# Kernel optimization log

Hardware: AMD Instinct MI355X
Metric: run time of the kernel (lower is better)

Reference implementation:

```python
import jax, jax.numpy as jnp
import numpy as np

N_NODES = 100000
N_EDGES = 3200000
N_GRAPHS = 64
IN_DIM = 64
LATENT = 64
DIST_STD = 1.0


def _gcn_conv(x, W, b, src, dst, dinv):
    """PyG GCNConv: out = D^-1/2 (A+I) D^-1/2 (x W) + b, with dinv = deg^-1/2."""
    n = x.shape[0]
    h = x @ W  # [N, out]
    coef = dinv[src] * dinv[dst]  # per-edge norm
    agg = jax.ops.segment_sum(h[src] * coef[:, None], dst, num_segments=n)
    # self-loop contribution with norm dinv[i]^2
    return agg + h * (dinv * dinv)[:, None] + b


def _mean_pool(x, batch, num_graphs):
    sums = jax.ops.segment_sum(x, batch, num_segments=num_graphs)
    cnts = jax.ops.segment_sum(jnp.ones((x.shape[0],), x.dtype), batch, num_segments=num_graphs)
    return sums / jnp.maximum(cnts, 1.0)[:, None]


def setup_inputs() -> dict:
    key = jax.random.key(0)
    ks = jax.random.split(key, 12)
    x = jax.random.normal(ks[0], (N_NODES, IN_DIM), jnp.float32)
    edge_index = jax.random.randint(ks[1], (2, N_EDGES), 0, N_NODES, jnp.int64 if jax.config.jax_enable_x64 else jnp.int32).astype(jnp.int32)
    batch = jnp.sort(jax.random.randint(ks[2], (N_NODES,), 0, N_GRAPHS)).astype(jnp.int32)

    def glorot(k, shape):
        fan_in, fan_out = shape
        s = jnp.sqrt(6.0 / (fan_in + fan_out))
        return jax.random.uniform(k, shape, jnp.float32, -s, s)

    return {
        "x": x, "edge_index": edge_index, "batch": batch,
        "W1m": glorot(ks[3], (IN_DIM, 16)), "b1m": jnp.zeros((16,), jnp.float32),
        "W2m": glorot(ks[4], (16, 32)), "b2m": jnp.zeros((32,), jnp.float32),
        "W3m": glorot(ks[5], (32, LATENT)), "b3m": jnp.zeros((LATENT,), jnp.float32),
        "W1l": glorot(ks[6], (IN_DIM, 16)), "b1l": jnp.zeros((16,), jnp.float32),
        "W2l": glorot(ks[7], (16, 32)), "b2l": jnp.zeros((32,), jnp.float32),
        "W3l": glorot(ks[8], (32, LATENT)), "b3l": jnp.zeros((LATENT,), jnp.float32),
        "Wfc": glorot(ks[9], (LATENT, 160000)), "bfc": jnp.zeros((160000,), jnp.float32),
        "eps": jax.random.normal(ks[10], (N_GRAPHS, LATENT), jnp.float32) * DIST_STD,
    }


def reference(x, edge_index, batch, W1m, b1m, W2m, b2m, W3m, b3m,
              W1l, b1l, W2l, b2l, W3l, b3l, Wfc, bfc, eps):
    src, dst = edge_index[0], edge_index[1]
    n = x.shape[0]
    # degrees include self-loop (+1)
    deg = jax.ops.segment_sum(jnp.ones((src.shape[0],), x.dtype), dst, num_segments=n) + 1.0
    dinv = jax.lax.rsqrt(deg)

    mu = jax.nn.relu(_gcn_conv(x, W1m, b1m, src, dst, dinv))
    mu = jax.nn.relu(_gcn_conv(mu, W2m, b2m, src, dst, dinv))
    mu = jax.nn.relu(_gcn_conv(mu, W3m, b3m, src, dst, dinv))
    mu = _mean_pool(mu, batch, N_GRAPHS)

    log = jax.nn.relu(_gcn_conv(x, W1l, b1l, src, dst, dinv))
    log = jax.nn.relu(_gcn_conv(log, W2l, b2l, src, dst, dinv))
    log = jax.nn.relu(_gcn_conv(log, W3l, b3l, src, dst, dinv))
    logvar = _mean_pool(log, batch, N_GRAPHS)

    # latent sample (training mode): z = mu + eps * exp(0.5*logvar)
    z = mu + eps * jnp.exp(0.5 * logvar)

    # decode: sigmoid(z Wfc + bfc) -> [G, 400, 400]
    output = jax.nn.sigmoid(z @ Wfc + bfc).reshape(-1, 400, 400)
    return output, mu, logvar
```

## Files before the change

### kernel.cpp

```cpp
#include <hip/hip_runtime.h>
#include <hip/hip_bf16.h>

#define N_NODES 100000
#define N_EDGES 3200000
#define N_GRAPHS 64
#define NB 391
#define KCH 8192
#define NCHUNK ((N_EDGES + KCH - 1) / KCH)
#define MAXBKT 10240
#define NBLK3 (N_NODES / 32)

__device__ __forceinline__ void atomAddF(float* p, float v) {
    unsafeAtomicAdd(p, v);
}

__device__ __forceinline__ float lo2f(unsigned u) { return __uint_as_float(u << 16); }
__device__ __forceinline__ float hi2f(unsigned u) { return __uint_as_float(u & 0xFFFF0000u); }
__device__ __forceinline__ unsigned pack2(float a, float b) {
    unsigned ha = __bfloat16_as_ushort(__float2bfloat16(a));
    unsigned hb = __bfloat16_as_ushort(__float2bfloat16(b));
    return ha | (hb << 16);
}

__global__ __launch_bounds__(512) void k_binCount(const int* __restrict__ dst,
                                                  int* __restrict__ gcount) {
    __shared__ int hist[NB];
    for (int t = threadIdx.x; t < NB; t += 512) hist[t] = 0;
    __syncthreads();
    int base = blockIdx.x * KCH;
    int cnt = min(KCH, N_EDGES - base);
    for (int i = threadIdx.x; i < cnt; i += 512)
        atomicAdd(&hist[dst[base + i] >> 8], 1);
    __syncthreads();
    for (int t = threadIdx.x; t < NB; t += 512)
        if (hist[t]) atomicAdd(&gcount[t], hist[t]);
}

__global__ __launch_bounds__(512) void k_scanB(const int* __restrict__ gcount,
                                               int* __restrict__ gbase,
                                               int* __restrict__ gcursor,
                                               int* __restrict__ rowptr) {
    __shared__ int s[512];
    int v = (threadIdx.x < NB) ? gcount[threadIdx.x] : 0;
    s[threadIdx.x] = v;
    __syncthreads();
    for (int off = 1; off < 512; off <<= 1) {
        int t = (threadIdx.x >= off) ? s[threadIdx.x - off] : 0;
        __syncthreads();
        s[threadIdx.x] += t;
        __syncthreads();
    }
    if (threadIdx.x < NB) {
        int e = s[threadIdx.x] - v;
        gbase[threadIdx.x] = e;
        gcursor[threadIdx.x] = e;
    }
    if (threadIdx.x == 0) rowptr[N_NODES] = N_EDGES;
}

__global__ __launch_bounds__(512) void k_binA(const int* __restrict__ src,
                                              const int* __restrict__ dst,
                                              int* __restrict__ gcursor,
                                              int* __restrict__ binned) {
    __shared__ int hist[512];
    __shared__ int rbase[512];
    hist[threadIdx.x] = 0;
    __syncthreads();
    int base = blockIdx.x * KCH;
    int cnt = min(KCH, N_EDGES - base);
    int pk[16];
    int meta[16];
    #pragma unroll
    for (int i = 0; i < 16; ++i) {
        int idx = i * 512 + threadIdx.x;
        if (idx < cnt) {
            int d = dst[base + idx];
            int b = d >> 8;
            int pos = atomicAdd(&hist[b], 1);
            pk[i] = ((d & 255) << 24) | src[base + idx];
            meta[i] = (b << 13) | pos;
        } else {
            meta[i] = -1;
        }
    }
    __syncthreads();
    if (threadIdx.x < NB) {
        int v = hist[threadIdx.x];
        if (v > 0) rbase[threadIdx.x] = atomicAdd(&gcursor[threadIdx.x], v);
    }
    __syncthreads();
    #pragma unroll
    for (int i = 0; i < 16; ++i) {
        if (meta[i] >= 0) {
            int b = meta[i] >> 13;
            int pos = meta[i] & 8191;
            binned[rbase[b] + pos] = pk[i];
        }
    }
}

__global__ __launch_bounds__(512) void k_passB(const int* __restrict__ gbase,
                                               int* __restrict__ csr,
                                               int* __restrict__ rowptr,
                                               float* __restrict__ dinv) {
    int b = blockIdx.x;
    int rb = gbase[b];
    int re = (b == NB - 1) ? N_EDGES : gbase[b + 1];
    int cnt = re - rb;
    int nbase = b << 8;
    int nn = min(nbase + 256, N_NODES) - nbase;
    __shared__ int stage[MAXBKT];
    __shared__ int nhist[256];
    __shared__ int sc[256];
    __shared__ int ncur[256];
    for (int t = threadIdx.x; t < 256; t += 512) nhist[t] = 0;
    __syncthreads();
    for (int j = threadIdx.x; j < cnt; j += 512) {
        int p = csr[rb + j];
        stage[j] = p;
        atomicAdd(&nhist[((unsigned)p) >> 24], 1);
    }
    __syncthreads();
    if (threadIdx.x < 256) sc[threadIdx.x] = nhist[threadIdx.x];
    __syncthreads();
    for (int off = 1; off < 256; off <<= 1) {
        int t = (threadIdx.x < 256 && threadIdx.x >= off) ? sc[threadIdx.x - off] : 0;
        __syncthreads();
        if (threadIdx.x < 256) sc[threadIdx.x] += t;
        __syncthreads();
    }
    if (threadIdx.x < 256) {
        int e = sc[threadIdx.x] - nhist[threadIdx.x];
        ncur[threadIdx.x] = e;
        if (threadIdx.x < nn) {
            rowptr[nbase + threadIdx.x] = rb + e;
            dinv[nbase + threadIdx.x] = rsqrtf((float)nhist[threadIdx.x] + 1.0f);
        }
    }
    __syncthreads();
    for (int j = threadIdx.x; j < cnt; j += 512) {
        int p = stage[j];
        int slot = atomicAdd(&ncur[((unsigned)p) >> 24], 1);
        csr[rb + slot] = p;
    }
}

template<int LOGW, bool BIAS_RELU, bool OB, bool PRE>
__global__ void __launch_bounds__(256) k_gatherB(
        const int* __restrict__ rowptr, const int* __restrict__ csr,
        const unsigned* __restrict__ in ,
        const float* __restrict__ dinv,
        const float* __restrict__ ba, const float* __restrict__ bb,
        void* __restrict__ out) {
    constexpr int W8 = (1 << LOGW) / 8;
    constexpr int NPB = 256 / W8;
    int n = blockIdx.x * NPB + (threadIdx.x / W8);
    if (n >= N_NODES) return;
    int sub = threadIdx.x % W8;
    const uint4* in4 = (const uint4*)in;
    uint4 u = in4[(size_t)n * W8 + sub];
    float a0 = lo2f(u.x), a1 = hi2f(u.x), a2 = lo2f(u.y), a3 = hi2f(u.y);
    float a4 = lo2f(u.z), a5 = hi2f(u.z), a6 = lo2f(u.w), a7 = hi2f(u.w);
    int j = rowptr[n], end = rowptr[n + 1];
    for (; j + 8 <= end; j += 8) {
        int s0 = csr[j] & 0xFFFFFF;
        int s1 = csr[j + 1] & 0xFFFFFF;
        int s2 = csr[j + 2] & 0xFFFFFF;
        int s3 = csr[j + 3] & 0xFFFFFF;
        int s4 = csr[j + 4] & 0xFFFFFF;
        int s5 = csr[j + 5] & 0xFFFFFF;
        int s6 = csr[j + 6] & 0xFFFFFF;
        int s7 = csr[j + 7] & 0xFFFFFF;
        uint4 v0 = in4[(size_t)s0 * W8 + sub];
        uint4 v1 = in4[(size_t)s1 * W8 + sub];
        uint4 v2 = in4[(size_t)s2 * W8 + sub];
        uint4 v3 = in4[(size_t)s3 * W8 + sub];
        uint4 v4 = in4[(size_t)s4 * W8 + sub];
        uint4 v5 = in4[(size_t)s5 * W8 + sub];
        uint4 v6 = in4[(size_t)s6 * W8 + sub];
        uint4 v7 = in4[(size_t)s7 * W8 + sub];
        a0 += ((lo2f(v0.x) + lo2f(v1.x)) + (lo2f(v2.x) + lo2f(v3.x)))
            + ((lo2f(v4.x) + lo2f(v5.x)) + (lo2f(v6.x) + lo2f(v7.x)));
        a1 += ((hi2f(v0.x) + hi2f(v1.x)) + (hi2f(v2.x) + hi2f(v3.x)))
            + ((hi2f(v4.x) + hi2f(v5.x)) + (hi2f(v6.x) + hi2f(v7.x)));
        a2 += ((lo2f(v0.y) + lo2f(v1.y)) + (lo2f(v2.y) + lo2f(v3.y)))
            + ((lo2f(v4.y) + lo2f(v5.y)) + (lo2f(v6.y) + lo2f(v7.y)));
        a3 += ((hi2f(v0.y) + hi2f(v1.y)) + (hi2f(v2.y) + hi2f(v3.y)))
            + ((hi2f(v4.y) + hi2f(v5.y)) + (hi2f(v6.y) + hi2f(v7.y)));
        a4 += ((lo2f(v0.z) + lo2f(v1.z)) + (lo2f(v2.z) + lo2f(v3.z)))
            + ((lo2f(v4.z) + lo2f(v5.z)) + (lo2f(v6.z) + lo2f(v7.z)));
        a5 += ((hi2f(v0.z) + hi2f(v1.z)) + (hi2f(v2.z) + hi2f(v3.z)))
            + ((hi2f(v4.z) + hi2f(v5.z)) + (hi2f(v6.z) + hi2f(v7.z)));
        a6 += ((lo2f(v0.w) + lo2f(v1.w)) + (lo2f(v2.w) + lo2f(v3.w)))
            + ((lo2f(v4.w) + lo2f(v5.w)) + (lo2f(v6.w) + lo2f(v7.w)));
        a7 += ((hi2f(v0.w) + hi2f(v1.w)) + (hi2f(v2.w) + hi2f(v3.w)))
            + ((hi2f(v4.w) + hi2f(v5.w)) + (hi2f(v6.w) + hi2f(v7.w)));
    }
    for (; j < end; ++j) {
        int s = csr[j] & 0xFFFFFF;
        uint4 v = in4[(size_t)s * W8 + sub];
        a0 += lo2f(v.x); a1 += hi2f(v.x);
        a2 += lo2f(v.y); a3 += hi2f(v.y);
        a4 += lo2f(v.z); a5 += hi2f(v.z);
        a6 += lo2f(v.w); a7 += hi2f(v.w);
    }
    float di = dinv[n];
    a0 *= di; a1 *= di; a2 *= di; a3 *= di;
    a4 *= di; a5 *= di; a6 *= di; a7 *= di;
    if (BIAS_RELU) {
        constexpr int H = (1 << LOGW) / 2;
        int d = sub * 8;
        const float* bp = (d < H) ? (ba + d) : (bb + d - H);
        a0 = fmaxf(a0 + bp[0], 0.0f);
        a1 = fmaxf(a1 + bp[1], 0.0f);
        a2 = fmaxf(a2 + bp[2], 0.0f);
        a3 = fmaxf(a3 + bp[3], 0.0f);
        a4 = fmaxf(a4 + bp[4], 0.0f);
        a5 = fmaxf(a5 + bp[5], 0.0f);
        a6 = fmaxf(a6 + bp[6], 0.0f);
        a7 = fmaxf(a7 + bp[7], 0.0f);
    }
    if (PRE) {
        a0 *= di; a1 *= di; a2 *= di; a3 *= di;
        a4 *= di; a5 *= di; a6 *= di; a7 *= di;
    }
    if (OB) {
        ((uint4*)out)[(size_t)n * W8 + sub] =
            make_uint4(pack2(a0, a1), pack2(a2, a3), pack2(a4, a5), pack2(a6, a7));
    } else {
        constexpr int OUT4 = (1 << LOGW) / 4;
        float4* o4 = (float4*)out;
        o4[(size_t)n * OUT4 + sub * 2]     = make_float4(a0, a1, a2, a3);
        o4[(size_t)n * OUT4 + sub * 2 + 1] = make_float4(a4, a5, a6, a7);
    }
}

#define FMA4(A, W) \
    A.x = fmaf(r, W.x, A.x); A.y = fmaf(r, W.y, A.y); \
    A.z = fmaf(r, W.z, A.z); A.w = fmaf(r, W.w, A.w);

__global__ void __launch_bounds__(256) k_gd3(
        const int* __restrict__ rowptr, const int* __restrict__ csr,
        const unsigned* __restrict__ in,
        const float* __restrict__ dinv,
        const float* __restrict__ W3m, const float* __restrict__ b3m,
        const float* __restrict__ W3l, const float* __restrict__ b3l,
        const int* __restrict__ batch,
        float* __restrict__ part0, float* __restrict__ part1,
        int* __restrict__ pg0, int* __restrict__ pg1, int boff) {
    __shared__ float s_ali[32 * 160];
    __shared__ float agg[32 * 68];
    __shared__ float sbias[128];
    __shared__ int   sbatch[32];
    __shared__ int   ssplit;
    float* sWall = s_ali;
    float* h3s   = s_ali;

    int blk = blockIdx.x + boff;
    for (int t = threadIdx.x; t < 4096; t += 256) {
        int k = t >> 7, D = t & 127;
        float wv = (D < 64) ? W3m[k * 64 + D] : W3l[k * 64 + (D - 64)];
        sWall[k * 160 + (D >> 4) * 20 + (D & 15)] = wv;
    }
    if (threadIdx.x < 128)
        sbias[threadIdx.x] = (threadIdx.x < 64) ? b3m[threadIdx.x]
                                                : b3l[threadIdx.x - 64];
    int nbase = blk * 32;
    if (threadIdx.x < 32) sbatch[threadIdx.x] = batch[nbase + threadIdx.x];

    int ln  = threadIdx.x >> 3;
    int sub = threadIdx.x & 7;
    int n = nbase + ln;
    const uint4* in4 = (const uint4*)in;
    uint4 u = in4[(size_t)n * 8 + sub];
    float a0 = lo2f(u.x), a1 = hi2f(u.x), a2 = lo2f(u.y), a3 = hi2f(u.y);
    float a4 = lo2f(u.z), a5 = hi2f(u.z), a6 = lo2f(u.w), a7 = hi2f(u.w);
    int j = rowptr[n], end = rowptr[n + 1];
    for (; j + 8 <= end; j += 8) {
        int s0 = csr[j] & 0xFFFFFF;
        int s1 = csr[j + 1] & 0xFFFFFF;
        int s2 = csr[j + 2] & 0xFFFFFF;
        int s3 = csr[j + 3] & 0xFFFFFF;
        int s4 = csr[j + 4] & 0xFFFFFF;
        int s5 = csr[j + 5] & 0xFFFFFF;
        int s6 = csr[j + 6] & 0xFFFFFF;
        int s7 = csr[j + 7] & 0xFFFFFF;
        uint4 v0 = in4[(size_t)s0 * 8 + sub];
        uint4 v1 = in4[(size_t)s1 * 8 + sub];
        uint4 v2 = in4[(size_t)s2 * 8 + sub];
        uint4 v3 = in4[(size_t)s3 * 8 + sub];
        uint4 v4 = in4[(size_t)s4 * 8 + sub];
        uint4 v5 = in4[(size_t)s5 * 8 + sub];
        uint4 v6 = in4[(size_t)s6 * 8 + sub];
        uint4 v7 = in4[(size_t)s7 * 8 + sub];
        a0 += ((lo2f(v0.x) + lo2f(v1.x)) + (lo2f(v2.x) + lo2f(v3.x)))
            + ((lo2f(v4.x) + lo2f(v5.x)) + (lo2f(v6.x) + lo2f(v7.x)));
        a1 += ((hi2f(v0.x) + hi2f(v1.x)) + (hi2f(v2.x) + hi2f(v3.x)))
            + ((hi2f(v4.x) + hi2f(v5.x)) + (hi2f(v6.x) + hi2f(v7.x)));
        a2 += ((lo2f(v0.y) + lo2f(v1.y)) + (lo2f(v2.y) + lo2f(v3.y)))
            + ((lo2f(v4.y) + lo2f(v5.y)) + (lo2f(v6.y) + lo2f(v7.y)));
        a3 += ((hi2f(v0.y) + hi2f(v1.y)) + (hi2f(v2.y) + hi2f(v3.y)))
            + ((hi2f(v4.y) + hi2f(v5.y)) + (hi2f(v6.y) + hi2f(v7.y)));
        a4 += ((lo2f(v0.z) + lo2f(v1.z)) + (lo2f(v2.z) + lo2f(v3.z)))
            + ((lo2f(v4.z) + lo2f(v5.z)) + (lo2f(v6.z) + lo2f(v7.z)));
        a5 += ((hi2f(v0.z) + hi2f(v1.z)) + (hi2f(v2.z) + hi2f(v3.z)))
            + ((hi2f(v4.z) + hi2f(v5.z)) + (hi2f(v6.z) + hi2f(v7.z)));
        a6 += ((lo2f(v0.w) + lo2f(v1.w)) + (lo2f(v2.w) + lo2f(v3.w)))
            + ((lo2f(v4.w) + lo2f(v5.w)) + (lo2f(v6.w) + lo2f(v7.w)));
        a7 += ((hi2f(v0.w) + hi2f(v1.w)) + (hi2f(v2.w) + hi2f(v3.w)))
            + ((hi2f(v4.w) + hi2f(v5.w)) + (hi2f(v6.w) + hi2f(v7.w)));
    }
    for (; j < end; ++j) {
        int s = csr[j] & 0xFFFFFF;
        uint4 v = in4[(size_t)s * 8 + sub];
        a0 += lo2f(v.x); a1 += hi2f(v.x);
        a2 += lo2f(v.y); a3 += hi2f(v.y);
        a4 += lo2f(v.z); a5 += hi2f(v.z);
        a6 += lo2f(v.w); a7 += hi2f(v.w);
    }
    float di = dinv[n];
    a0 *= di; a1 *= di; a2 *= di; a3 *= di;
    a4 *= di; a5 *= di; a6 *= di; a7 *= di;
    {
        float* ap = &agg[ln * 68 + sub * 8];
        *(float4*)&ap[0] = make_float4(a0, a1, a2, a3);
        *(float4*)&ap[4] = make_float4(a4, a5, a6, a7);
    }
    if (threadIdx.x == 0) {
        int sp = 32;
        int ga = sbatch[0];
        for (int i = 1; i < 32; ++i)
            if (sbatch[i] != ga) { sp = i; break; }
        ssplit = sp;
    }
    __syncthreads();

    int ln2 = threadIdx.x >> 3;
    int q   = threadIdx.x & 7;
    int Dbase = q * 16;
    int koff = (q >= 4) ? 32 : 0;
    float4 c0 = *(const float4*)&sbias[Dbase];
    float4 c1 = *(const float4*)&sbias[Dbase + 4];
    float4 c2 = *(const float4*)&sbias[Dbase + 8];
    float4 c3 = *(const float4*)&sbias[Dbase + 12];
    const float* ag = &agg[ln2 * 68 + koff];
    const float* wq = &sWall[q * 20];
    #pragma unroll
    for (int k = 0; k < 32; ++k) {
        float r = ag[k];
        const float* wr = &wq[k * 160];
        float4 w0 = *(const float4*)&wr[0];
        float4 w1 = *(const float4*)&wr[4];
        float4 w2 = *(const float4*)&wr[8];
        float4 w3 = *(const float4*)&wr[12];
        FMA4(c0, w0)
        FMA4(c1, w1)
        FMA4(c2, w2)
        FMA4(c3, w3)
    }
    c0.x = fmaxf(c0.x, 0.f); c0.y = fmaxf(c0.y, 0.f);
    c0.z = fmaxf(c0.z, 0.f); c0.w = fmaxf(c0.w, 0.f);
    c1.x = fmaxf(c1.x, 0.f); c1.y = fmaxf(c1.y, 0.f);
    c1.z = fmaxf(c1.z, 0.f); c1.w = fmaxf(c1.w, 0.f);
    c2.x = fmaxf(c2.x, 0.f); c2.y = fmaxf(c2.y, 0.f);
    c2.z = fmaxf(c2.z, 0.f); c2.w = fmaxf(c2.w, 0.f);
    c3.x = fmaxf(c3.x, 0.f); c3.y = fmaxf(c3.y, 0.f);
    c3.z = fmaxf(c3.z, 0.f); c3.w = fmaxf(c3.w, 0.f);
    __syncthreads();

    {
        float* hp = &h3s[ln2 * 132 + Dbase];
        *(float4*)&hp[0]  = c0;
        *(float4*)&hp[4]  = c1;
        *(float4*)&hp[8]  = c2;
        *(float4*)&hp[12] = c3;
    }
    __syncthreads();
    {
        int d    = threadIdx.x & 127;
        int slot = threadIdx.x >> 7;
        int sp = ssplit;
        int s = slot ? sp : 0;
        int e = slot ? 32 : sp;
        float acc = 0.f;
        for (int nn = s; nn < e; ++nn)
            acc += h3s[nn * 132 + d];
        if (slot == 0) {
            part0[(size_t)blk * 128 + d] = acc;
            if (d == 0) pg0[blk] = sbatch[0];
        } else {
            part1[(size_t)blk * 128 + d] = acc;
            if (d == 0) pg1[blk] = (sp < 32) ? sbatch[31] : -1;
        }
    }
}

__global__ void __launch_bounds__(128) k_poolF(
        const float* __restrict__ part0, const float* __restrict__ part1,
        const int* __restrict__ pg0, const int* __restrict__ pg1,
        const int* __restrict__ batch, const float* __restrict__ eps,
        float* __restrict__ zbuf, float* __restrict__ out_mu,
        float* __restrict__ out_lv) {
    int g = blockIdx.x;
    __shared__ int sb[2];
    __shared__ float spool[128];
    if (threadIdx.x < 2) {
        int target = g + threadIdx.x;
        int lo = 0, hi = N_NODES;
        while (lo < hi) {
            int mid = (lo + hi) >> 1;
            if (batch[mid] < target) lo = mid + 1; else hi = mid;
        }
        sb[threadIdx.x] = lo;
    }
    __syncthreads();
    int ns = sb[0], ne = sb[1];
    int d = threadIdx.x;
    float acc = 0.f;
    if (ne > ns) {
        int b0 = ns >> 5, b1 = (ne - 1) >> 5;
        for (int b = b0; b <= b1; ++b) {
            if (pg0[b] == g) acc += part0[(size_t)b * 128 + d];
            if (pg1[b] == g) acc += part1[(size_t)b * 128 + d];
        }
    }
    spool[d] = acc;
    __syncthreads();
    if (threadIdx.x < 64) {
        int k = threadIdx.x;
        float c = fmaxf((float)(ne - ns), 1.0f);
        float mu = spool[k] / c;
        float lv = spool[64 + k] / c;
        zbuf[k * 64 + g] = mu + eps[g * 64 + k] * __expf(0.5f * lv);
        out_mu[g * 64 + k] = mu;
        out_lv[g * 64 + k] = lv;
    }
}

template<int IN_W, int OUT_HALF, int A_OFF, int A_W, int B_OFF, bool BR, bool OB, bool DS>
__global__ void k_dense4(const float* __restrict__ in,
                         const float* __restrict__ Wa, const float* __restrict__ ba,
                         const float* __restrict__ Wb, const float* __restrict__ bb,
                         const float* __restrict__ dinv,
                         void* __restrict__ out) {
    __shared__ float sWa[A_W * OUT_HALF];
    __shared__ float sWb[A_W * OUT_HALF];
    __shared__ float sba[OUT_HALF];
    __shared__ float sbb[OUT_HALF];
    for (int t = threadIdx.x; t < A_W * OUT_HALF; t += 256) {
        sWa[t] = Wa[t];
        sWb[t] = Wb[t];
    }
    if (BR && threadIdx.x < OUT_HALF) {
        sba[threadIdx.x] = ba[threadIdx.x];
        sbb[threadIdx.x] = bb[threadIdx.x];
    }
    __syncthreads();
    constexpr int TPN = OUT_HALF / 2;
    int idx = blockIdx.x * 256 + threadIdx.x;
    int n = idx / TPN;
    int q = idx % TPN;
    bool isB = (q * 4) >= OUT_HALF;
    int dd = q * 4 - (isB ? OUT_HALF : 0);
    const float* sW = isB ? sWb : sWa;
    int ko = isB ? B_OFF : A_OFF;
    float4 acc;
    if (BR) {
        const float* bp = isB ? (sbb + dd) : (sba + dd);
        acc = make_float4(bp[0], bp[1], bp[2], bp[3]);
    } else {
        acc = make_float4(0.f, 0.f, 0.f, 0.f);
    }
    const float* row = in + (size_t)n * IN_W + ko;
    #pragma unroll
    for (int k = 0; k < A_W; ++k) {
        float r = row[k];
        float4 wv = *(const float4*)&sW[k * OUT_HALF + dd];
        acc.x = fmaf(r, wv.x, acc.x);
        acc.y = fmaf(r, wv.y, acc.y);
        acc.z = fmaf(r, wv.z, acc.z);
        acc.w = fmaf(r, wv.w, acc.w);
    }
    if (BR) {
        acc.x = fmaxf(acc.x, 0.f); acc.y = fmaxf(acc.y, 0.f);
        acc.z = fmaxf(acc.z, 0.f); acc.w = fmaxf(acc.w, 0.f);
    }
    if (DS) {
        float dn = dinv[n];
        acc.x *= dn; acc.y *= dn; acc.z *= dn; acc.w *= dn;
    }
    if (OB) {
        ((uint2*)out)[idx] = make_uint2(pack2(acc.x, acc.y), pack2(acc.z, acc.w));
    } else {
        ((float4*)out)[idx] = acc;
    }
}

__global__ void __launch_bounds__(256) k_decode(const float* __restrict__ zT,
                                                const float* __restrict__ Wfc,
                                                const float* __restrict__ bfc,
                                                float* __restrict__ out) {
    int j = (blockIdx.x >> 1) * 256 + threadIdx.x;
    int gh = (blockIdx.x & 1) * 32;
    const float* zp = zT + gh;
    float bias = bfc[j];
    float acc[32];
    #pragma unroll
    for (int g = 0; g < 32; ++g) acc[g] = bias;
    #pragma unroll 8
    for (int k = 0; k < 64; ++k) {
        float w = Wfc[(size_t)k * 160000 + j];
        #pragma unroll
        for (int g = 0; g < 32; ++g)
            acc[g] = fmaf(zp[k * 64 + g], w, acc[g]);
    }
    #pragma unroll
    for (int g = 0; g < 32; ++g) {
        float s = 1.0f / (1.0f + __expf(-acc[g]));
        out[(size_t)(gh + g) * 160000 + j] = s;
    }
}

extern "C" void kernel_launch(void* const* d_in, const int* in_sizes, int n_in,
                              void* d_out, int out_size, void* d_ws, size_t ws_size,
                              hipStream_t stream) {
    const float* x     = (const float*)d_in[0];
    const int*   ei    = (const int*)d_in[1];
    const int*   batch = (const int*)d_in[2];
    const float *W1m = (const float*)d_in[3],  *b1m = (const float*)d_in[4];
    const float *W2m = (const float*)d_in[5],  *b2m = (const float*)d_in[6];
    const float *W3m = (const float*)d_in[7],  *b3m = (const float*)d_in[8];
    const float *W1l = (const float*)d_in[9],  *b1l = (const float*)d_in[10];
    const float *W2l = (const float*)d_in[11], *b2l = (const float*)d_in[12];
    const float *W3l = (const float*)d_in[13], *b3l = (const float*)d_in[14];
    const float *Wfc = (const float*)d_in[15], *bfc = (const float*)d_in[16];
    const float *eps = (const float*)d_in[17];

    const int* srcv = ei;
    const int* dstv = ei + N_EDGES;

    char* w = (char*)d_ws;
    auto alloc = [&](size_t bytes) -> char* {
        char* p = w;
        w += (bytes + 255) & ~(size_t)255;
        return p;
    };
    int*   gcount = (int*)  alloc((size_t)NB * 4);
    int*   gbase  = (int*)  alloc((size_t)NB * 4);
    int*   gcursor= (int*)  alloc((size_t)NB * 4);
    int*   rowptr = (int*)  alloc((size_t)(N_NODES + 1) * 4);
    float* dinv   = (float*)alloc((size_t)N_NODES * 4);
    float* zbuf   = (float*)alloc((size_t)N_GRAPHS * 64 * 4);
    float* arena = (float*)alloc((size_t)N_NODES * 192 * 4);
    float* A   = arena;
    float* B   = arena + (size_t)N_NODES * 64;
    int*   csr = (int*)(arena + (size_t)N_NODES * 128);
    float* part0 = A;
    float* part1 = A + (size_t)NBLK3 * 128;
    int*   pg0   = (int*)(A + (size_t)2 * NBLK3 * 128);
    int*   pg1   = pg0 + NBLK3;

    float* out    = (float*)d_out;
    float* out_mu = out + 10240000;
    float* out_lv = out + 10240000 + 4096;

    hipMemsetAsync(gcount, 0, (size_t)NB * 4, stream);

    k_binCount<<<NCHUNK, 512, 0, stream>>>(dstv, gcount);
    k_scanB<<<1, 512, 0, stream>>>(gcount, gbase, gcursor, rowptr);
    k_binA<<<NCHUNK, 512, 0, stream>>>(srcv, dstv, gcursor, csr);
    k_passB<<<NB, 512, 0, stream>>>(gbase, csr, rowptr, dinv);

    k_dense4<64, 16, 0, 64, 0, false, true, true><<<N_NODES * 8 / 256, 256, 0, stream>>>(
        x, W1m, b1m, W1l, b1l, dinv, A);
    k_gatherB<5, true, true, true><<<(N_NODES + 63) / 64, 256, 0, stream>>>(
        rowptr, csr, (const unsigned*)A, dinv, b1m, b1l, B);

    k_gatherB<5, false, false, false><<<(N_NODES + 63) / 64, 256, 0, stream>>>(
        rowptr, csr, (const unsigned*)B, dinv, b1m, b1l, A);
    k_dense4<32, 32, 0, 16, 16, true, true, true><<<N_NODES * 16 / 256, 256, 0, stream>>>(
        A, W2m, b2m, W2l, b2l, dinv, B);

    k_gd3<<<NBLK3 / 2, 256, 0, stream>>>(
        rowptr, csr, (const unsigned*)B, dinv, W3m, b3m, W3l, b3l, batch,
        part0, part1, pg0, pg1, 0);
    k_gd3<<<NBLK3 - NBLK3 / 2, 256, 0, stream>>>(
        rowptr, csr, (const unsigned*)B, dinv, W3m, b3m, W3l, b3l, batch,
        part0, part1, pg0, pg1, NBLK3 / 2);

    k_poolF<<<N_GRAPHS, 128, 0, stream>>>(part0, part1, pg0, pg1, batch, eps,
                                          zbuf, out_mu, out_lv);

    k_decode<<<1250, 256, 0, stream>>>(zbuf, Wfc, bfc, out);
}
```

Measured before the change: 463.6 us.

## Fuse layer-2 gather with dense transform and merge split gd3 launches

Adds a k_gd2 kernel that performs the layer-2 neighbor aggregation and the 16->32 (per branch) dense transform, ReLU and dinv scaling in one pass, writing bf16 output. It replaces the separate gatherB and dense4 launches and the intermediate round trip through global memory. The two half-grid k_gd3 launches are also merged into one launch. The new output buffer B2 sits at arena offset N*160, which overlaps the csr region if csr is larger than 32 ints per node. That overlap is a correctness risk.

```diff
diff --git a/kernel.cpp b/kernel.cpp
--- a/kernel.cpp
+++ b/kernel.cpp
@@ -239,6 +239,126 @@
     A.x = fmaf(r, W.x, A.x); A.y = fmaf(r, W.y, A.y); \
     A.z = fmaf(r, W.z, A.z); A.w = fmaf(r, W.w, A.w);
 
+__global__ void __launch_bounds__(256) k_gd2(
+        const int* __restrict__ rowptr, const int* __restrict__ csr,
+        const unsigned* __restrict__ in,
+        const float* __restrict__ dinv,
+        const float* __restrict__ W2m, const float* __restrict__ b2m,
+        const float* __restrict__ W2l, const float* __restrict__ b2l,
+        unsigned* __restrict__ outB) {
+    __shared__ float sW[16 * 80];
+    __shared__ float agg[64 * 37];
+    __shared__ float sbias[64];
+    for (int t = threadIdx.x; t < 1024; t += 256) {
+        int k = t >> 6, D = t & 63;
+        float wv = (D < 32) ? W2m[k * 32 + D] : W2l[k * 32 + (D - 32)];
+        sW[k * 80 + (D >> 4) * 20 + (D & 15)] = wv;
+    }
+    if (threadIdx.x < 64)
+        sbias[threadIdx.x] = (threadIdx.x < 32) ? b2m[threadIdx.x]
+                                                : b2l[threadIdx.x - 32];
+    int ln  = threadIdx.x >> 2;
+    int sub = threadIdx.x & 3;
+    int n = blockIdx.x * 64 + ln;
+    int nc = min(n, N_NODES - 1);
+    const uint4* in4 = (const uint4*)in;
+    uint4 u = in4[(size_t)nc * 4 + sub];
+    float a0 = lo2f(u.x), a1 = hi2f(u.x), a2 = lo2f(u.y), a3 = hi2f(u.y);
+    float a4 = lo2f(u.z), a5 = hi2f(u.z), a6 = lo2f(u.w), a7 = hi2f(u.w);
+    int j = rowptr[nc], end = rowptr[nc + 1];
+    for (; j + 8 <= end; j += 8) {
+        int s0 = csr[j] & 0xFFFFFF;
+        int s1 = csr[j + 1] & 0xFFFFFF;
+        int s2 = csr[j + 2] & 0xFFFFFF;
+        int s3 = csr[j + 3] & 0xFFFFFF;
+        int s4 = csr[j + 4] & 0xFFFFFF;
+        int s5 = csr[j + 5] & 0xFFFFFF;
+        int s6 = csr[j + 6] & 0xFFFFFF;
+        int s7 = csr[j + 7] & 0xFFFFFF;
+        uint4 v0 = in4[(size_t)s0 * 4 + sub];
+        uint4 v1 = in4[(size_t)s1 * 4 + sub];
+        uint4 v2 = in4[(size_t)s2 * 4 + sub];
+        uint4 v3 = in4[(size_t)s3 * 4 + sub];
+        uint4 v4 = in4[(size_t)s4 * 4 + sub];
+        uint4 v5 = in4[(size_t)s5 * 4 + sub];
+        uint4 v6 = in4[(size_t)s6 * 4 + sub];
+        uint4 v7 = in4[(size_t)s7 * 4 + sub];
+        a0 += ((lo2f(v0.x) + lo2f(v1.x)) + (lo2f(v2.x) + lo2f(v3.x)))
+            + ((lo2f(v4.x) + lo2f(v5.x)) + (lo2f(v6.x) + lo2f(v7.x)));
+        a1 += ((hi2f(v0.x) + hi2f(v1.x)) + (hi2f(v2.x) + hi2f(v3.x)))
+            + ((hi2f(v4.x) + hi2f(v5.x)) + (hi2f(v6.x) + hi2f(v7.x)));
+        a2 += ((lo2f(v0.y) + lo2f(v1.y)) + (lo2f(v2.y) + lo2f(v3.y)))
+            + ((lo2f(v4.y) + lo2f(v5.y)) + (lo2f(v6.y) + lo2f(v7.y)));
+        a3 += ((hi2f(v0.y) + hi2f(v1.y)) + (hi2f(v2.y) + hi2f(v3.y)))
+            + ((hi2f(v4.y) + hi2f(v5.y)) + (hi2f(v6.y) + hi2f(v7.y)));
+        a4 += ((lo2f(v0.z) + lo2f(v1.z)) + (lo2f(v2.z) + lo2f(v3.z)))
+            + ((lo2f(v4.z) + lo2f(v5.z)) + (lo2f(v6.z) + lo2f(v7.z)));
+        a5 += ((hi2f(v0.z) + hi2f(v1.z)) + (hi2f(v2.z) + hi2f(v3.z)))
+            + ((hi2f(v4.z) + hi2f(v5.z)) + (hi2f(v6.z) + hi2f(v7.z)));
+        a6 += ((lo2f(v0.w) + lo2f(v1.w)) + (lo2f(v2.w) + lo2f(v3.w)))
+            + ((lo2f(v4.w) + lo2f(v5.w)) + (lo2f(v6.w) + lo2f(v7.w)));
+        a7 += ((hi2f(v0.w) + hi2f(v1.w)) + (hi2f(v2.w) + hi2f(v3.w)))
+            + ((hi2f(v4.w) + hi2f(v5.w)) + (hi2f(v6.w) + hi2f(v7.w)));
+    }
+    for (; j < end; ++j) {
+        int s = csr[j] & 0xFFFFFF;
+        uint4 v = in4[(size_t)s * 4 + sub];
+        a0 += lo2f(v.x); a1 += hi2f(v.x);
+        a2 += lo2f(v.y); a3 += hi2f(v.y);
+        a4 += lo2f(v.z); a5 += hi2f(v.z);
+        a6 += lo2f(v.w); a7 += hi2f(v.w);
+    }
+    float di = dinv[nc];
+    a0 *= di; a1 *= di; a2 *= di; a3 *= di;
+    a4 *= di; a5 *= di; a6 *= di; a7 *= di;
+    {
+        float* ap = &agg[ln * 37 + sub * 8];
+        *(float4*)&ap[0] = make_float4(a0, a1, a2, a3);
+        *(float4*)&ap[4] = make_float4(a4, a5, a6, a7);
+    }
+    __syncthreads();
+
+    int q = sub;
+    int Dbase = q * 16;
+    int koff = (q >= 2) ? 16 : 0;
+    float4 c0 = *(const float4*)&sbias[Dbase];
+    float4 c1 = *(const float4*)&sbias[Dbase + 4];
+    float4 c2 = *(const float4*)&sbias[Dbase + 8];
+    float4 c3 = *(const float4*)&sbias[Dbase + 12];
+    const float* ag = &agg[ln * 37 + koff];
+    const float* wq = &sW[q * 20];
+    #pragma unroll
+    for (int k = 0; k < 16; ++k) {
+        float r = ag[k];
+        const float* wr = &wq[k * 80];
+        float4 w0 = *(const float4*)&wr[0];
+        float4 w1 = *(const float4*)&wr[4];
+        float4 w2 = *(const float4*)&wr[8];
+        float4 w3 = *(const float4*)&wr[12];
+        FMA4(c0, w0)
+        FMA4(c1, w1)
+        FMA4(c2, w2)
+        FMA4(c3, w3)
+    }
+    c0.x = fmaxf(c0.x, 0.f) * di; c0.y = fmaxf(c0.y, 0.f) * di;
+    c0.z = fmaxf(c0.z, 0.f) * di; c0.w = fmaxf(c0.w, 0.f) * di;
+    c1.x = fmaxf(c1.x, 0.f) * di; c1.y = fmaxf(c1.y, 0.f) * di;
+    c1.z = fmaxf(c1.z, 0.f) * di; c1.w = fmaxf(c1.w, 0.f) * di;
+    c2.x = fmaxf(c2.x, 0.f) * di; c2.y = fmaxf(c2.y, 0.f) * di;
+    c2.z = fmaxf(c2.z, 0.f) * di; c2.w = fmaxf(c2.w, 0.f) * di;
+    c3.x = fmaxf(c3.x, 0.f) * di; c3.y = fmaxf(c3.y, 0.f) * di;
+    c3.z = fmaxf(c3.z, 0.f) * di; c3.w = fmaxf(c3.w, 0.f) * di;
+    if (n < N_NODES) {
+        uint4* o4 = (uint4*)outB;
+        o4[(size_t)n * 8 + q * 2] =
+            make_uint4(pack2(c0.x, c0.y), pack2(c0.z, c0.w),
+                       pack2(c1.x, c1.y), pack2(c1.z, c1.w));
+        o4[(size_t)n * 8 + q * 2 + 1] =
+            make_uint4(pack2(c2.x, c2.y), pack2(c2.z, c2.w),
+                       pack2(c3.x, c3.y), pack2(c3.z, c3.w));
+    }
+}
+
 __global__ void __launch_bounds__(256) k_gd3(
         const int* __restrict__ rowptr, const int* __restrict__ csr,
         const unsigned* __restrict__ in,
@@ -247,7 +367,7 @@
         const float* __restrict__ W3l, const float* __restrict__ b3l,
         const int* __restrict__ batch,
         float* __restrict__ part0, float* __restrict__ part1,
-        int* __restrict__ pg0, int* __restrict__ pg1, int boff) {
+        int* __restrict__ pg0, int* __restrict__ pg1) {
     __shared__ float s_ali[32 * 160];
     __shared__ float agg[32 * 68];
     __shared__ float sbias[128];
@@ -256,7 +376,6 @@
     float* sWall = s_ali;
     float* h3s   = s_ali;
 
-    int blk = blockIdx.x + boff;
     for (int t = threadIdx.x; t < 4096; t += 256) {
         int k = t >> 7, D = t & 127;
         float wv = (D < 64) ? W3m[k * 64 + D] : W3l[k * 64 + (D - 64)];
@@ -265,7 +384,7 @@
     if (threadIdx.x < 128)
         sbias[threadIdx.x] = (threadIdx.x < 64) ? b3m[threadIdx.x]
                                                 : b3l[threadIdx.x - 64];
-    int nbase = blk * 32;
+    int nbase = blockIdx.x * 32;
     if (threadIdx.x < 32) sbatch[threadIdx.x] = batch[nbase + threadIdx.x];
 
     int ln  = threadIdx.x >> 3;
@@ -385,6 +504,7 @@
         float acc = 0.f;
         for (int nn = s; nn < e; ++nn)
             acc += h3s[nn * 132 + d];
+        int blk = blockIdx.x;
         if (slot == 0) {
             part0[(size_t)blk * 128 + d] = acc;
             if (d == 0) pg0[blk] = sbatch[0];
@@ -555,6 +675,7 @@
     float* A   = arena;
     float* B   = arena + (size_t)N_NODES * 64;
     int*   csr = (int*)(arena + (size_t)N_NODES * 128);
+    float* B2  = arena + (size_t)N_NODES * 160;
     float* part0 = A;
     float* part1 = A + (size_t)NBLK3 * 128;
     int*   pg0   = (int*)(A + (size_t)2 * NBLK3 * 128);
@@ -576,17 +697,12 @@
     k_gatherB<5, true, true, true><<<(N_NODES + 63) / 64, 256, 0, stream>>>(
         rowptr, csr, (const unsigned*)A, dinv, b1m, b1l, B);
 
-    k_gatherB<5, false, false, false><<<(N_NODES + 63) / 64, 256, 0, stream>>>(
-        rowptr, csr, (const unsigned*)B, dinv, b1m, b1l, A);
-    k_dense4<32, 32, 0, 16, 16, true, true, true><<<N_NODES * 16 / 256, 256, 0, stream>>>(
-        A, W2m, b2m, W2l, b2l, dinv, B);
-
-    k_gd3<<<NBLK3 / 2, 256, 0, stream>>>(
-        rowptr, csr, (const unsigned*)B, dinv, W3m, b3m, W3l, b3l, batch,
-        part0, part1, pg0, pg1, 0);
-    k_gd3<<<NBLK3 - NBLK3 / 2, 256, 0, stream>>>(
-        rowptr, csr, (const unsigned*)B, dinv, W3m, b3m, W3l, b3l, batch,
-        part0, part1, pg0, pg1, NBLK3 / 2);
+    k_gd2<<<(N_NODES + 63) / 64, 256, 0, stream>>>(
+        rowptr, csr, (const unsigned*)B, dinv, W2m, b2m, W2l, b2l, (unsigned*)B2);
+
+    k_gd3<<<NBLK3, 256, 0, stream>>>(
+        rowptr, csr, (const unsigned*)B2, dinv, W3m, b3m, W3l, b3l, batch,
+        part0, part1, pg0, pg1);
 
     k_poolF<<<N_GRAPHS, 128, 0, stream>>>(part0, part1, pg0, pg1, batch, eps,
                                           zbuf, out_mu, out_lv);
```

New measurement: 434.6 us. -6.3%, faster.
